# Kernel tuning notes

Hardware: AMD Instinct MI355X
Metric: run time of the kernel (lower is better)

The kernel has to match this reference:

```python
import jax, jax.numpy as jnp
import numpy as np

# (multiplicity, dim=2l+1) per irreducible field, for both input and output
RS = [(8, 1), (8, 3), (8, 5)]
SIZE = 3          # conv kernel spatial size
B_EL = 2          # radial basis elements per (i,j) kernel block
EPS = 1e-5


def _se3_bn_conv(x, weight, bases):
    """Training-mode SE3BatchNorm stats fused into dynamic kernel build + conv3d.
    x: (B, C_in, D, H, W); weight: flat (sum mi*mj*b_el,);
    bases[i][j]: (b_el, di, dj, SIZE, SIZE, SIZE).
    """
    B = x.shape[0]
    means = []    # per scalar (d==1) field: (m,)
    scales = []   # per field: (m,) inverse-std factors
    ix = 0
    for m, d in RS:
        field = x[:, ix:ix + m * d].reshape(B, m, d, -1)
        ix += m * d
        if d == 1:
            mean = jax.lax.stop_gradient(field.mean(axis=-1).mean(axis=0).reshape(-1))
            field = field - mean.reshape(1, m, 1, 1)
            means.append(mean)
        # reduce='mean': sum over d, mean over spatial, mean over batch (detached)
        norm = jax.lax.stop_gradient(jnp.sum(field * field, axis=2).mean(axis=-1).mean(axis=0))
        scales.append((norm + EPS) ** -0.5)

    # Build normalized dynamic kernel blocks and compensating bias
    widx = 0
    row_blocks = []
    bias_parts = []
    for i, (mi, di) in enumerate(RS):
        col_blocks = []
        bia = jnp.zeros((mi * di,), x.dtype)
        imean = 0
        for j, (mj, dj) in enumerate(RS):
            basis = bases[i][j]                     # (b, di, dj, s, s, s)
            b = basis.shape[0]
            w = weight[widx:widx + mi * mj * b].reshape(mi, mj, b)
            widx += mi * mj * b
            w = w * scales[j][None, :, None]        # per-input-field BN rescale
            # block: (mi*di, mj*dj, s, s, s)
            block = jnp.einsum('uvb,bdexyz->udvexyz', w, basis)
            col_blocks.append(block.reshape(mi * di, mj * dj, SIZE, SIZE, SIZE))
            if di == 1 and dj == 1:
                mean = means[imean]
                imean += 1
                identity = basis.reshape(b, -1).sum(-1)         # (b,)
                corr = (w.reshape(-1, b) @ identity[:, None]).reshape(mi, mj)
                bia = bia - (corr @ mean[:, None]).reshape(-1)
        row_blocks.append(jnp.concatenate(col_blocks, axis=1))
        bias_parts.append(bia)
    kernel = jnp.concatenate(row_blocks, axis=0)    # (C_out, C_in, s, s, s)
    bias = jnp.concatenate(bias_parts)              # (C_out,)

    out = jax.lax.conv_general_dilated(
        x, kernel, window_strides=(1, 1, 1), padding='VALID',
        dimension_numbers=('NCDHW', 'OIDHW', 'NCDHW'))
    return out + bias[None, :, None, None, None]


def setup_inputs() -> dict:
    key = jax.random.key(0)
    k_x, k_w = jax.random.split(key)
    C = sum(m * d for m, d in RS)  # 72
    x = jax.random.normal(k_x, (8, C, 32, 32, 32), jnp.float32)
    total_w = sum(mi * mj * B_EL for mi, _ in RS for mj, _ in RS)  # 1152
    weight = jax.random.normal(k_w, (total_w,), jnp.float32) * 0.1
    inp = {'x': x, 'weight': weight}
    for i, (mi, di) in enumerate(RS):
        for j, (mj, dj) in enumerate(RS):
            kb = jax.random.fold_in(key, 100 + 10 * i + j)
            inp['basis_{}_{}'.format(i, j)] = jax.random.normal(
                kb, (B_EL, di, dj, SIZE, SIZE, SIZE), jnp.float32) / (SIZE ** 1.5)
    return inp


def reference(x, weight, basis_0_0, basis_0_1, basis_0_2,
              basis_1_0, basis_1_1, basis_1_2,
              basis_2_0, basis_2_1, basis_2_2):
    bases = [[basis_0_0, basis_0_1, basis_0_2],
             [basis_1_0, basis_1_1, basis_1_2],
             [basis_2_0, basis_2_1, basis_2_2]]
    return _se3_bn_conv(x, weight, bases)
```

## Files before the change

### kernel.cpp

```cpp
#include <hip/hip_runtime.h>
#include <hip/hip_fp16.h>
#include <math.h>

#define NCH 72
#define SP  32768
#define NBATCH 8
#define NTOT (NBATCH*SP)

#define WS_SUMX   0
#define WS_SUMSQ  72
#define WS_SCALE  144
#define WS_BIAS   216
#define WS_K      288

#define WS_XH_BYTES 323712
#define XH_ROW   2720
#define XH_PLANE 87040
#define XH_BATCH 2785280

typedef __attribute__((ext_vector_type(8))) _Float16 half8;
typedef __attribute__((ext_vector_type(4))) float float4v;
typedef __attribute__((ext_vector_type(4))) int int4v;

__device__ __forceinline__ void chmap(int c, int& f, int& m, int& d, int& dim) {
  if (c < 8)       { f = 0; m = c;          d = 0;          dim = 1; }
  else if (c < 32) { f = 1; m = (c - 8)/3;  d = (c - 8)%3;  dim = 3; }
  else             { f = 2; m = (c - 32)/5; d = (c - 32)%5; dim = 5; }
}

__global__ __launch_bounds__(256) void prepack_kernel(const float* __restrict__ x,
                                                      float* __restrict__ ws) {
  __shared__ __align__(16) short tile[256 * 88];
  __shared__ float segS[72][3], segQ[72][3];
  const int t    = threadIdx.x;
  const int z    = blockIdx.x >> 1;
  const int half = blockIdx.x & 1;
  const int b    = blockIdx.y;
  ushort* xh = (ushort*)((char*)ws + WS_XH_BYTES);
  const float* xb = x + (size_t)b * NCH * SP + z * 1024 + half * 512;

  const int ci_s = t % 72, seg = t / 72;
  float accS = 0.f, accQ = 0.f;

  *(int4v*)&tile[t * 88 + 72] = (int4v){0, 0, 0, 0};

  for (int c = 0; c < 2; ++c) {
    if (c) __syncthreads();
    #pragma unroll
    for (int cig = 0; cig < 18; ++cig) {
      float v0 = xb[(size_t)(cig*4 + 0) * SP + c * 256 + t];
      float v1 = xb[(size_t)(cig*4 + 1) * SP + c * 256 + t];
      float v2 = xb[(size_t)(cig*4 + 2) * SP + c * 256 + t];
      float v3 = xb[(size_t)(cig*4 + 3) * SP + c * 256 + t];
      short s4[4] = { (short)__half_as_short(__float2half(v0)),
                      (short)__half_as_short(__float2half(v1)),
                      (short)__half_as_short(__float2half(v2)),
                      (short)__half_as_short(__float2half(v3)) };
      *(int2*)&tile[t * 88 + cig * 4] = *(const int2*)s4;
    }
    __syncthreads();
    {
      ushort* gb = xh + (size_t)b * XH_BATCH + (size_t)(z * 32 + (half * 2 + c) * 8) * XH_ROW;
      #pragma unroll
      for (int j = 0; j < 10; ++j) {
        const int s   = t + j * 256;
        const int pos = s / 10, part = s - pos * 10;
        const int4v v = *(const int4v*)&tile[pos * 88 + part * 8];
        const int row = pos >> 5, xx = pos & 31;
        *(int4v*)(gb + (size_t)row * XH_ROW + xx * 80 + part * 8) = v;
      }
    }
    if (seg < 3) {
      const int p0 = seg * 86;
      const int pn = (seg == 2) ? 84 : 86;
      for (int i = 0; i < pn; ++i) {
        const float v = __half2float(__short_as_half(tile[(p0 + i) * 88 + ci_s]));
        accS += v; accQ += v * v;
      }
    }
  }
  if (seg < 3) { segS[ci_s][seg] = accS; segQ[ci_s][seg] = accQ; }
  __syncthreads();
  if (t < 144) {
    const int which = t / 72, ci = t % 72;
    const float v = which ? (segQ[ci][0] + segQ[ci][1] + segQ[ci][2])
                          : (segS[ci][0] + segS[ci][1] + segS[ci][2]);
    atomicAdd(&ws[(which ? WS_SUMSQ : WS_SUMX) + ci], v);
  }
}

__global__ __launch_bounds__(256) void build_half_kernel(const float* __restrict__ weight,
    float* __restrict__ ws,
    const float* __restrict__ b00, const float* __restrict__ b01, const float* __restrict__ b02,
    const float* __restrict__ b10, const float* __restrict__ b11, const float* __restrict__ b12,
    const float* __restrict__ b20, const float* __restrict__ b21, const float* __restrict__ b22) {
  const int tid = blockIdx.x * 256 + threadIdx.x;
  const float invN = 1.0f / (float)NTOT;
  if (tid < 315 * 512) {
    const int blk = tid >> 9;
    const int e   = tid & 511;
    const int tap = blk / 35;
    const int r   = blk - tap * 35;
    const int kc  = r / 5, cj = r - (r / 5) * 5;
    const int l   = e >> 3, j = e & 7;
    const int co  = cj * 16 + (l & 15);
    const int kk  = kc * 32 + ((l >> 4) << 3) + j;
    short val = 0;
    if (co < NCH && kk < 216) {
      const int dx = kk / 72, ci = kk - dx * 72;
      int fi, u, dd, di; chmap(co, fi, u, dd, di);
      int fj, v, ee, dj; chmap(ci, fj, v, ee, dj);
      const float* bs[9] = {b00, b01, b02, b10, b11, b12, b20, b21, b22};
      const float* basis = bs[fi * 3 + fj];
      float norm;
      if (ci < 8) {
        float m = ws[WS_SUMX + ci] * invN;
        norm = ws[WS_SUMSQ + ci] * invN - m * m;
      } else if (ci < 32) {
        int m0 = 8 + ((ci - 8) / 3) * 3;
        norm = (ws[WS_SUMSQ+m0] + ws[WS_SUMSQ+m0+1] + ws[WS_SUMSQ+m0+2]) * invN;
      } else {
        int m0 = 32 + ((ci - 32) / 5) * 5;
        norm = (ws[WS_SUMSQ+m0] + ws[WS_SUMSQ+m0+1] + ws[WS_SUMSQ+m0+2]
              + ws[WS_SUMSQ+m0+3] + ws[WS_SUMSQ+m0+4]) * invN;
      }
      const float sc = 1.0f / sqrtf(norm + 1e-5f);
      const float* wp = weight + (fi * 3 + fj) * 128 + (u * 8 + v) * 2;
      const float w0 = wp[0] * sc, w1 = wp[1] * sc;
      const int t = tap * 3 + dx;
      const float f = w0 * basis[(dd * dj + ee) * 27 + t]
                    + w1 * basis[((di + dd) * dj + ee) * 27 + t];
      val = __half_as_short(__float2half(f));
    }
    ((short*)(ws + WS_K))[tid] = val;
  }
  if (blockIdx.x == 0) {
    __shared__ float s_mean[8], s_scale[8];
    const int c = threadIdx.x;
    if (c < 8) {
      float m = ws[WS_SUMX + c] * invN;
      float norm = ws[WS_SUMSQ + c] * invN - m * m;
      s_mean[c]  = m;
      s_scale[c] = 1.0f / sqrtf(norm + 1e-5f);
    }
    __syncthreads();
    if (c < NCH) {
      float bia = 0.f;
      if (c < 8) {
        float id0 = 0.f, id1 = 0.f;
        #pragma unroll
        for (int t = 0; t < 27; ++t) { id0 += b00[t]; id1 += b00[27 + t]; }
        #pragma unroll
        for (int v = 0; v < 8; ++v) {
          float s  = s_scale[v];
          float w0 = weight[(c*8 + v)*2 + 0] * s;
          float w1 = weight[(c*8 + v)*2 + 1] * s;
          bia -= (w0 * id0 + w1 * id1) * s_mean[v];
        }
      }
      ws[WS_BIAS + c] = bia;
    }
  }
}

__global__ __launch_bounds__(256, 2) void conv_direct(const float* __restrict__ ws,
                                                      float* __restrict__ out) {
  extern __shared__ __align__(16) char Bsm[];

  const int lane = threadIdx.x & 63;
  const int wv   = threadIdx.x >> 6;
  const int lx   = lane & 15;
  const int q    = lane >> 4;
  const int i  = blockIdx.x;
  const int b  = i & 7;
  const int q2 = i >> 3;
  const int yt = q2 & 7;
  const int zp = q2 >> 3;
  const int y  = yt * 4 + wv;
  const int yc = (y > 29) ? 29 : y;
  const int zb = zp * 2;

  const char* xhb = (const char*)ws + WS_XH_BYTES + (size_t)b * (XH_BATCH * 2);
  const char* Kb  = (const char*)(ws + WS_K);
  const float* __restrict__ bias = ws + WS_BIAS;

  const int lb16 = lane * 16;

  float4v acc[2][2][5];
  #pragma unroll
  for (int sz = 0; sz < 2; ++sz)
    #pragma unroll
    for (int s = 0; s < 2; ++s)
      #pragma unroll
      for (int cj = 0; cj < 5; ++cj)
        acc[sz][s][cj] = (float4v){0.f, 0.f, 0.f, 0.f};

#define STAGE(TAP, BUF) {                                                         \
    const char* src_ = Kb + (size_t)(TAP) * 35840;                                \
    char* dst_ = Bsm + (size_t)(BUF) * 35840;                                     \
    _Pragma("unroll")                                                             \
    for (int k = 0; k < 9; ++k) {                                                 \
      const int idx = (int)threadIdx.x + (k << 8);                                \
      if (idx < 2240) {                                                           \
        __builtin_amdgcn_global_load_lds(                                         \
          (const __attribute__((address_space(1))) void*)(src_ + (size_t)idx*16), \
          (__attribute__((address_space(3))) void*)(dst_ + ((k<<8) + (wv<<6))*16),\
          16, 0, 0);                                                              \
      }                                                                           \
    }                                                                             \
  }

#define LOADA(R0, R1, KC, A) {                                                    \
    const int kk0_ = (KC) * 32 + (q << 3);                                        \
    const int dx_  = (kk0_ >= 144) ? 2 : ((kk0_ >= 72) ? 1 : 0);                  \
    const int ao_  = (lx * 80 + kk0_ + 8 * dx_) * 2;                              \
    A[0] = *(const half8*)((R0) + ao_);                                           \
    A[1] = *(const half8*)((R0) + ao_ + 2560);                                    \
    A[2] = *(const half8*)((R1) + ao_);                                           \
    A[3] = *(const half8*)((R1) + ao_ + 2560);                                    \
  }

#define BPRE(BC, KC, BQ) {                                                        \
    BQ[0] = *(const half8*)((BC) + ((KC)*5 + 0)*1024 + lb16);                     \
    BQ[1] = *(const half8*)((BC) + ((KC)*5 + 1)*1024 + lb16);                     \
    BQ[2] = *(const half8*)((BC) + ((KC)*5 + 2)*1024 + lb16);                     \
    BQ[3] = *(const half8*)((BC) + ((KC)*5 + 3)*1024 + lb16);                     \
    BQ[4] = *(const half8*)((BC) + ((KC)*5 + 4)*1024 + lb16);                     \
  }

#define MFQ(A, BF, CJ)                                                                         \
    acc[0][0][CJ] = __builtin_amdgcn_mfma_f32_16x16x32_f16(A[0], BF, acc[0][0][CJ], 0,0,0);    \
    acc[0][1][CJ] = __builtin_amdgcn_mfma_f32_16x16x32_f16(A[1], BF, acc[0][1][CJ], 0,0,0);    \
    acc[1][0][CJ] = __builtin_amdgcn_mfma_f32_16x16x32_f16(A[2], BF, acc[1][0][CJ], 0,0,0);    \
    acc[1][1][CJ] = __builtin_amdgcn_mfma_f32_16x16x32_f16(A[3], BF, acc[1][1][CJ], 0,0,0);

#define MFMAG(A, BQ) {                                                            \
    __builtin_amdgcn_s_setprio(1);                                                \
    MFQ(A, BQ[0], 0) MFQ(A, BQ[1], 1) MFQ(A, BQ[2], 2) MFQ(A, BQ[3], 3) MFQ(A, BQ[4], 4) \
    __builtin_amdgcn_s_setprio(0);                                                \
  }

#define TAPBODY(TT, X, Y, Z) {                                                    \
    const int T_  = (TT);                                                         \
    const int dz_ = T_ / 3, dy_ = T_ - 3 * dz_;                                   \
    const char* r0T = xhb + (size_t)(((zb + dz_) * 32) + (yc + dy_)) * (XH_ROW*2);\
    const char* r1T = r0T + (XH_PLANE * 2);                                       \
    const char* Bc  = Bsm + (size_t)(T_ & 1) * 35840;                             \
    BPRE(Bc, 0, Bq0);                                                             \
    if (T_ < 8) STAGE(T_ + 1, ((T_ + 1) & 1));                                    \
    const int Tn_  = (T_ < 8) ? T_ + 1 : T_;                                      \
    const int dzn_ = Tn_ / 3, dyn_ = Tn_ - 3 * dzn_;                              \
    const char* rn0 = xhb + (size_t)(((zb + dzn_) * 32) + (yc + dyn_)) * (XH_ROW*2);\
    const char* rn1 = rn0 + (XH_PLANE * 2);                                       \
    BPRE(Bc, 1, Bq1); LOADA(r0T, r1T, 2, Z);  MFMAG(X, Bq0);                      \
    BPRE(Bc, 2, Bq0); LOADA(r0T, r1T, 3, X);  MFMAG(Y, Bq1);                      \
    BPRE(Bc, 3, Bq1); LOADA(r0T, r1T, 4, Y);  MFMAG(Z, Bq0);                      \
    BPRE(Bc, 4, Bq0); LOADA(r0T, r1T, 5, Z);  MFMAG(X, Bq1);                      \
    BPRE(Bc, 5, Bq1); LOADA(r0T, r1T, 6, X);  MFMAG(Y, Bq0);                      \
    BPRE(Bc, 6, Bq0); if (T_ < 8) LOADA(rn0, rn1, 0, Y);  MFMAG(Z, Bq1);          \
    if (T_ < 8) LOADA(rn0, rn1, 1, Z);  MFMAG(X, Bq0);                            \
    if (T_ < 8) {                                                                 \
      asm volatile("s_waitcnt vmcnt(8)" ::: "memory");                            \
      __builtin_amdgcn_s_barrier();                                               \
    }                                                                             \
  }

  half8 A0[4], A1[4], A2[4], Bq0[5], Bq1[5];

  STAGE(0, 0);
  {
    const char* r0P = xhb + (size_t)((zb * 32) + yc) * (XH_ROW * 2);
    const char* r1P = r0P + (XH_PLANE * 2);
    LOADA(r0P, r1P, 0, A0);
    LOADA(r0P, r1P, 1, A1);
  }
  asm volatile("s_waitcnt vmcnt(8)" ::: "memory");
  __builtin_amdgcn_s_barrier();

  #pragma unroll 1
  for (int s3 = 0; s3 < 9; s3 += 3) {
    TAPBODY(s3 + 0, A0, A1, A2)
    TAPBODY(s3 + 1, A1, A2, A0)
    TAPBODY(s3 + 2, A2, A0, A1)
  }

#undef STAGE
#undef LOADA
#undef BPRE
#undef MFQ
#undef MFMAG
#undef TAPBODY

  if (y < 30) {
    #pragma unroll
    for (int cj = 0; cj < 5; ++cj) {
      const int co = cj * 16 + lx;
      if (co < NCH) {
        const float bv = bias[co];
        #pragma unroll
        for (int sz = 0; sz < 2; ++sz) {
          float* ob = out + ((size_t)(b * NCH + co) * 30 + (zb + sz)) * 900 + y * 30;
          #pragma unroll
          for (int s = 0; s < 2; ++s) {
            const int x0 = s * 16 + q * 4;
            const float4v v = acc[sz][s][cj];
            float2 p0; p0.x = v[0] + bv; p0.y = v[1] + bv;
            *(float2*)(ob + x0) = p0;
            if (x0 + 2 < 30) {
              float2 p1; p1.x = v[2] + bv; p1.y = v[3] + bv;
              *(float2*)(ob + x0 + 2) = p1;
            }
          }
        }
      }
    }
  }
}

extern "C" void kernel_launch(void* const* d_in, const int* in_sizes, int n_in,
                              void* d_out, int out_size, void* d_ws, size_t ws_size,
                              hipStream_t stream) {
  const float* x = (const float*)d_in[0];
  const float* w = (const float*)d_in[1];
  const float* bs[9];
  for (int i = 0; i < 9; ++i) bs[i] = (const float*)d_in[2 + i];
  float* ws  = (float*)d_ws;
  float* out = (float*)d_out;

  hipMemsetAsync(d_ws, 0, 144 * sizeof(float), stream);

  prepack_kernel<<<dim3(64, NBATCH), 256, 0, stream>>>(x, ws);
  build_half_kernel<<<(315 * 512 + 255) / 256, 256, 0, stream>>>(
      w, ws, bs[0], bs[1], bs[2], bs[3], bs[4], bs[5], bs[6], bs[7], bs[8]);
  conv_direct<<<dim3(960), 256, 71680, stream>>>(ws, out);
}
```

Baseline: 255.9 us.

## Store packed fp16 input row-planar by channel group to coalesce stores and A loads

The prepacked fp16 activation layout changes from position-major (80 halves per x position) to channel-group-major: each row holds 10 groups of 8 channels laid out across 34 x positions. The prepack write becomes a direct strided store per channel group with explicit zero padding. The conv A-fragment loads use precomputed per-k-chunk offsets into the new layout. Smaller tweaks remove the per-thread pointer array for basis selection and unroll the stats loop. The new layout aims for contiguous lane accesses (16 lanes read adjacent x positions within one group), but the producer and consumer must agree exactly on strides and padding, and those regions are only partly visible.

Measured after the change: 234.6 us. 1.09x faster.

```diff
diff --git a/kernel.cpp b/kernel.cpp
--- a/kernel.cpp
+++ b/kernel.cpp
@@ -41,8 +41,6 @@
 
   const int ci_s = t % 72, seg = t / 72;
   float accS = 0.f, accQ = 0.f;
-
-  *(int4v*)&tile[t * 88 + 72] = (int4v){0, 0, 0, 0};
 
   for (int c = 0; c < 2; ++c) {
     if (c) __syncthreads();
@@ -62,17 +60,23 @@
     {
       ushort* gb = xh + (size_t)b * XH_BATCH + (size_t)(z * 32 + (half * 2 + c) * 8) * XH_ROW;
       #pragma unroll
-      for (int j = 0; j < 10; ++j) {
-        const int s   = t + j * 256;
-        const int pos = s / 10, part = s - pos * 10;
-        const int4v v = *(const int4v*)&tile[pos * 88 + part * 8];
-        const int row = pos >> 5, xx = pos & 31;
-        *(int4v*)(gb + (size_t)row * XH_ROW + xx * 80 + part * 8) = v;
+      for (int j = 0; j < 9; ++j) {
+        const int4v v = *(const int4v*)&tile[t * 88 + j * 8];
+        *(int4v*)(gb + (size_t)(t >> 5) * XH_ROW + j * 272 + (t & 31) * 8) = v;
+      }
+      {
+        const int4v zz = (int4v){0, 0, 0, 0};
+        int idx = t;
+        *(int4v*)(gb + (size_t)(idx / 34) * XH_ROW + 9 * 272 + (idx % 34) * 8) = zz;
+        idx = 256 + t;
+        if (idx < 272)
+          *(int4v*)(gb + (size_t)(idx / 34) * XH_ROW + 9 * 272 + (idx % 34) * 8) = zz;
       }
     }
     if (seg < 3) {
       const int p0 = seg * 86;
       const int pn = (seg == 2) ? 84 : 86;
+      #pragma unroll 4
       for (int i = 0; i < pn; ++i) {
         const float v = __half2float(__short_as_half(tile[(p0 + i) * 88 + ci_s]));
         accS += v; accQ += v * v;
@@ -110,8 +114,16 @@
       const int dx = kk / 72, ci = kk - dx * 72;
       int fi, u, dd, di; chmap(co, fi, u, dd, di);
       int fj, v, ee, dj; chmap(ci, fj, v, ee, dj);
-      const float* bs[9] = {b00, b01, b02, b10, b11, b12, b20, b21, b22};
-      const float* basis = bs[fi * 3 + fj];
+      const int s9 = fi * 3 + fj;
+      const float* basis = b00;
+      if (s9 == 1) basis = b01;
+      if (s9 == 2) basis = b02;
+      if (s9 == 3) basis = b10;
+      if (s9 == 4) basis = b11;
+      if (s9 == 5) basis = b12;
+      if (s9 == 6) basis = b20;
+      if (s9 == 7) basis = b21;
+      if (s9 == 8) basis = b22;
       float norm;
       if (ci < 8) {
         float m = ws[WS_SUMX + ci] * invN;
@@ -125,7 +137,7 @@
               + ws[WS_SUMSQ+m0+3] + ws[WS_SUMSQ+m0+4]) * invN;
       }
       const float sc = 1.0f / sqrtf(norm + 1e-5f);
-      const float* wp = weight + (fi * 3 + fj) * 128 + (u * 8 + v) * 2;
+      const float* wp = weight + s9 * 128 + (u * 8 + v) * 2;
       const float w0 = wp[0] * sc, w1 = wp[1] * sc;
       const int t = tap * 3 + dx;
       const float f = w0 * basis[(dd * dj + ee) * 27 + t]
@@ -186,6 +198,13 @@
 
   const int lb16 = lane * 16;
 
+  int aoffb[7];
+  #pragma unroll
+  for (int kc = 0; kc < 7; ++kc) {
+    const int g = kc * 4 + q;
+    aoffb[kc] = ((g >= 27) ? 9 * 544 : (g % 9) * 544 + (g / 9) * 16) + lx * 16;
+  }
+
   float4v acc[2][2][5];
   #pragma unroll
   for (int sz = 0; sz < 2; ++sz)
@@ -211,13 +230,11 @@
   }
 
 #define LOADA(R0, R1, KC, A) {                                                    \
-    const int kk0_ = (KC) * 32 + (q << 3);                                        \
-    const int dx_  = (kk0_ >= 144) ? 2 : ((kk0_ >= 72) ? 1 : 0);                  \
-    const int ao_  = (lx * 80 + kk0_ + 8 * dx_) * 2;                              \
+    const int ao_ = aoffb[KC];                                                    \
     A[0] = *(const half8*)((R0) + ao_);                                           \
-    A[1] = *(const half8*)((R0) + ao_ + 2560);                                    \
+    A[1] = *(const half8*)((R0) + ao_ + 256);                                     \
     A[2] = *(const half8*)((R1) + ao_);                                           \
-    A[3] = *(const half8*)((R1) + ao_ + 2560);                                    \
+    A[3] = *(const half8*)((R1) + ao_ + 256);                                     \
   }
 
 #define BPRE(BC, KC, BQ) {                                                        \
```
